# Kernel optimization log

Measured on AMD Instinct MI355X. Metric: run time of the kernel, lower is better.

The kernel has to match this reference:

```python
import jax, jax.numpy as jnp
import numpy as np

H = 4096          # hidden_size
I = 11008         # intermediate_size
G = 128           # AWQ group_size
# AWQ interleaved nibble order within each packed int32
_ORDER = jnp.array([0, 4, 1, 5, 2, 6, 3, 7], dtype=jnp.int32) * 4


def _mk_lin(key, K, N):
    k1, k2, k3 = jax.random.split(key, 3)
    qw = jax.random.randint(k1, (K, N // 8), 0, 100, dtype=jnp.int32)
    qz = jax.random.randint(k2, (K // G, N // 8), 0, 100, dtype=jnp.int32)
    sc = jax.random.normal(k3, (K // G, N), dtype=jnp.float32) * 0.02
    return qw, qz, sc


def setup_inputs() -> dict:
    key = jax.random.key(0)
    ks = jax.random.split(key, 7)
    x = jax.random.normal(ks[0], (8, 16, H), dtype=jnp.float32)
    ln1_w = jnp.ones((H,), dtype=jnp.float32)
    ln2_w = jnp.ones((H,), dtype=jnp.float32)
    qkv_qw, qkv_qz, qkv_sc = _mk_lin(ks[1], H, 3 * H)
    o_qw, o_qz, o_sc = _mk_lin(ks[2], H, H)
    gu_qw, gu_qz, gu_sc = _mk_lin(ks[3], H, 2 * I)
    dn_qw, dn_qz, dn_sc = _mk_lin(ks[4], I, H)
    return dict(x=x, ln1_w=ln1_w, ln2_w=ln2_w,
                qkv_qw=qkv_qw, qkv_qz=qkv_qz, qkv_sc=qkv_sc,
                o_qw=o_qw, o_qz=o_qz, o_sc=o_sc,
                gu_qw=gu_qw, gu_qz=gu_qz, gu_sc=gu_sc,
                dn_qw=dn_qw, dn_qz=dn_qz, dn_sc=dn_sc)


def rmsnorm(x, w, eps=1e-6):
    return x * jax.lax.rsqrt(jnp.mean(x * x, axis=-1, keepdims=True) + eps) * w


def dequant(qw, qz, sc):
    # qw: [K, N//8] int32 -> [K, N]; qz: [K//G, N//8] -> [K//G, N]
    K = qw.shape[0]
    N = sc.shape[1]
    w = ((qw[:, :, None] >> _ORDER) & 0xF).reshape(K, N).astype(sc.dtype)
    z = ((qz[:, :, None] >> _ORDER) & 0xF).reshape(K // G, N).astype(sc.dtype)
    return (w - jnp.repeat(z, G, axis=0)) * jnp.repeat(sc, G, axis=0)


def lite_linear(x, qw, qz, sc):
    return x @ dequant(qw, qz, sc)


def reference(x, ln1_w, ln2_w,
              qkv_qw, qkv_qz, qkv_sc,
              o_qw, o_qz, o_sc,
              gu_qw, gu_qz, gu_sc,
              dn_qw, dn_qz, dn_sc):
    residual = x
    h = rmsnorm(x, ln1_w)
    h = lite_linear(h, qkv_qw, qkv_qz, qkv_sc)[..., :H]  # mock attn: take q slice
    h = lite_linear(h, o_qw, o_qz, o_sc)
    h = residual + h
    residual = h
    h = rmsnorm(h, ln2_w)
    gate_up = lite_linear(h, gu_qw, gu_qz, gu_sc)
    gate, up = gate_up[..., :I], gate_up[..., I:]
    h = lite_linear(jax.nn.silu(gate) * up, dn_qw, dn_qz, dn_sc)
    return residual + h
```

## Files before the change

### kernel.cpp

```cpp
#include <hip/hip_runtime.h>

typedef unsigned int   u32;
typedef unsigned short u16;

typedef _Float16 h2  __attribute__((ext_vector_type(2)));
typedef _Float16 h8  __attribute__((ext_vector_type(8)));
typedef float    f32x4 __attribute__((ext_vector_type(4)));

#define M_TOK 128

__device__ __forceinline__ u16 f2h_(float f) {
    _Float16 h = (_Float16)f; return __builtin_bit_cast(u16, h);
}
__device__ __forceinline__ float h2f_(u16 b) {
    _Float16 h = __builtin_bit_cast(_Float16, b); return (float)h;
}
__device__ __forceinline__ void acc8(uint4 v, float* s) {
#pragma unroll
    for (int i = 0; i < 4; ++i) {
        u32 w = ((const u32*)&v)[i];
        s[2 * i]     += h2f_((u16)(w & 0xFFFF));
        s[2 * i + 1] += h2f_((u16)(w >> 16));
    }
}

__constant__ int SHC[8] = {0, 16, 4, 20, 8, 24, 12, 28};

__launch_bounds__(256)
__global__ void pack_zs(const int* __restrict__ qz, const float* __restrict__ sc,
                        u32* __restrict__ zs, int qws, int scs, int Ncols, int total) {
    const int idx = blockIdx.x * 256 + threadIdx.x;
    if (idx >= total) return;
    const int g = idx / Ncols, n = idx - g * Ncols;
    const u32 d = (u32)qz[(size_t)g * qws + (n >> 3)];
    const u32 zj = (d >> SHC[n & 7]) & 15u;
    const u32 mz = 0xE400u | zj;
    const u16 sh = f2h_(sc[(size_t)g * scs + n]);
    zs[(size_t)g * Ncols + n] = mz | ((u32)sh << 16);
}


__launch_bounds__(256)
__global__ void rmsnorm_k(const float* __restrict__ in, const float* __restrict__ w,
                          u16* __restrict__ out) {
    const int row = blockIdx.x;
    const float* x = in + (size_t)row * 4096;
    float ss = 0.f;
#pragma unroll
    for (int j = 0; j < 16; ++j) {
        float v = x[threadIdx.x + 256 * j];
        ss += v * v;
    }
#pragma unroll
    for (int off = 32; off > 0; off >>= 1) ss += __shfl_down(ss, off, 64);
    __shared__ float ws4[4];
    if ((threadIdx.x & 63) == 0) ws4[threadIdx.x >> 6] = ss;
    __syncthreads();
    float total = ws4[0] + ws4[1] + ws4[2] + ws4[3];
    float r = rsqrtf(total * (1.f / 4096.f) + 1e-6f);
    const int mt = row >> 4, l16 = row & 15;
#pragma unroll
    for (int c2 = 0; c2 < 2; ++c2) {
        int c = threadIdx.x * 2 + c2;
        int kb = c >> 2, qq = c & 3;
        u16 o8[8];
#pragma unroll
        for (int j = 0; j < 8; ++j) {
            int i = c * 8 + j;
            o8[j] = f2h_(x[i] * r * w[i]);
        }
        *(uint4*)(out + ((size_t)(kb * 8 + mt) * 64 + qq * 16 + l16) * 8) = *(const uint4*)o8;
    }
}

__launch_bounds__(256, 3)
__global__ void gemm_awq(const u16* __restrict__ A, const u32* __restrict__ zs,
                         const int* __restrict__ qw, u16* __restrict__ part,
                         int qws, int N, int K, int kchunk) {
    __shared__ __align__(16) char ldsB[4 * 9216];

    const int tid = threadIdx.x, w = tid >> 6, lane = tid & 63;
    const int q = lane >> 4, l16 = lane & 15;
    const int nwg = gridDim.x, bid = blockIdx.x;
    const int qq8 = nwg >> 3, r8 = nwg & 7, xcd = bid & 7, boff = bid >> 3;
    const int bx = (xcd < r8 ? xcd * (qq8 + 1) : r8 * (qq8 + 1) + (xcd - r8) * qq8) + boff;
    const int n0w = bx * 128 + w * 32;
    const int pc0 = n0w >> 3;
    const int kp = lane & 31, h = lane >> 5;
    const int sk = blockIdx.y, kc0 = sk * kchunk, kend = min(kc0 + kchunk, K);

    char* buf0 = ldsB + w * 9216;
    char* buf1 = buf0 + 4608;
    const u16* Ala = A + lane * 8;
    const int* qws_base = qw + pc0;
    const u32* zsA = zs + n0w + h * 8;
    const u32* zsB = zs + n0w + 16 + h * 8;

    f32x4 acc[8][2] = {};
    uint4 za0, za1, zb0, zb1;

    auto ldraw = [&](int k0) -> uint4 {
        return *(const uint4*)(qws_base + (size_t)(k0 + lane) * qws);
    };
    auto loadzs = [&](int g) {
        za0 = *(const uint4*)(zsA + (size_t)g * N);
        za1 = *(const uint4*)(zsA + (size_t)g * N + 4);
        zb0 = *(const uint4*)(zsB + (size_t)g * N);
        zb1 = *(const uint4*)(zsB + (size_t)g * N + 4);
    };
    auto dq = [&](uint4 rv, char* buf) {
        const int i0 = kp * 8, i1 = i0 + 4;
        int b00 = __builtin_amdgcn_ds_bpermute(i0, (int)rv.x);
        int b10 = __builtin_amdgcn_ds_bpermute(i0, (int)rv.y);
        int b20 = __builtin_amdgcn_ds_bpermute(i0, (int)rv.z);
        int b30 = __builtin_amdgcn_ds_bpermute(i0, (int)rv.w);
        int b01 = __builtin_amdgcn_ds_bpermute(i1, (int)rv.x);
        int b11 = __builtin_amdgcn_ds_bpermute(i1, (int)rv.y);
        int b21 = __builtin_amdgcn_ds_bpermute(i1, (int)rv.z);
        int b31 = __builtin_amdgcn_ds_bpermute(i1, (int)rv.w);
        u32 qd0 = (u32)(h ? b10 : b00);
        u32 qd1 = (u32)(h ? b11 : b01);
        u32 qd2 = (u32)(h ? b30 : b20);
        u32 qd3 = (u32)(h ? b31 : b21);
        auto emit8 = [&](u32 w0, u32 w1, int nb, uint4 z0, uint4 z1) {
            char* bb = buf + kp * 4 + nb * 144;
            u32 w0s = w0 >> 4, w1s = w1 >> 4;
            auto em = [&](int j, u32 a0, u32 a1, int b, u32 zsj) {
                h2 mz = __builtin_bit_cast(h2, __builtin_amdgcn_perm(zsj, zsj, 0x01000100u));
                h2 s2 = __builtin_bit_cast(h2, __builtin_amdgcn_perm(zsj, zsj, 0x03020302u));
                u32 t = __builtin_amdgcn_perm(a1, a0, (u32)(b | ((b + 4) << 16)));
                u32 u = (t & 0x000F000Fu) | 0x64006400u;
                h2 v = (__builtin_bit_cast(h2, u) + mz) * s2;
                *(u32*)(bb + j * 144) = __builtin_bit_cast(u32, v);
            };
            em(0, w0, w1, 0, z0.x);  em(4, w0, w1, 1, z1.x);
            em(1, w0, w1, 2, z0.y);  em(5, w0, w1, 3, z1.y);
            em(2, w0s, w1s, 0, z0.z); em(6, w0s, w1s, 1, z1.z);
            em(3, w0s, w1s, 2, z0.w); em(7, w0s, w1s, 3, z1.w);
        };
        emit8(qd0, qd1, h * 8, za0, za1);
        emit8(qd2, qd3, 16 + h * 8, zb0, zb1);
    };

    uint4 rv_n = {0, 0, 0, 0};

    loadzs(kc0 >> 7);
    uint4 rv0 = ldraw(kc0);
    if (kc0 + 64 < kend) rv_n = ldraw(kc0 + 64);
    dq(rv0, buf0);
    if (((kc0 + 64) & 127) == 0 && kc0 + 64 < kend)
        loadzs((kc0 + 64) >> 7);

    char* cur = buf0; char* nxt = buf1;
    for (int k0 = kc0; k0 < kend; k0 += 64) {
        const bool kn1 = (k0 + 64) < kend, kn2 = (k0 + 128) < kend;
        uint4 rv_f = {0, 0, 0, 0};
        if (kn2) rv_f = ldraw(k0 + 128);
        if (kn1) dq(rv_n, nxt);
        if (kn2 && (((k0 + 128) & 127) == 0))
            loadzs((k0 + 128) >> 7);
        const int kb = k0 >> 5;
#pragma unroll
        for (int c = 0; c < 2; ++c) {
            uint4 bvc[2];
#pragma unroll
            for (int nt = 0; nt < 2; ++nt)
                bvc[nt] = *(const uint4*)(cur + (nt * 16 + l16) * 144 + c * 64 + q * 16);
            uint4 afc[8];
#pragma unroll
            for (int mt = 0; mt < 8; ++mt)
                afc[mt] = *(const uint4*)(Ala + (size_t)((kb + c) * 8 + mt) * 512);
#pragma unroll
            for (int mt = 0; mt < 8; ++mt)
#pragma unroll
                for (int nt = 0; nt < 2; ++nt)
                    acc[mt][nt] = __builtin_amdgcn_mfma_f32_16x16x32_f16(
                        __builtin_bit_cast(h8, afc[mt]),
                        __builtin_bit_cast(h8, bvc[nt]),
                        acc[mt][nt], 0, 0, 0);
        }
        rv_n = rv_f;
        char* t = cur; cur = nxt; nxt = t;
    }

    u16* pp = part + (size_t)sk * M_TOK * N;
#pragma unroll
    for (int mt = 0; mt < 8; ++mt)
#pragma unroll
        for (int nt = 0; nt < 2; ++nt) {
            const int n = n0w + nt * 16 + l16;
#pragma unroll
            for (int r = 0; r < 4; ++r) {
                const int m = mt * 16 + q * 4 + r;
                pp[(size_t)m * N + n] = f2h_(acc[mt][nt][r]);
            }
        }
}

__launch_bounds__(256)
__global__ void reduce_to_afrag(const u16* __restrict__ part, u16* __restrict__ out,
                                int SK) {
    const int idx = blockIdx.x * 256 + threadIdx.x;
    const int m = idx >> 9, c = idx & 511;
    float s[8] = {};
    for (int k = 0; k < SK; ++k)
        acc8(*(const uint4*)(part + (size_t)k * 524288 + (size_t)m * 4096 + c * 8), s);
    const int kb = c >> 2, qq = c & 3, mt = m >> 4, l16 = m & 15;
    u16 o8[8];
#pragma unroll
    for (int j = 0; j < 8; ++j) o8[j] = f2h_(s[j]);
    *(uint4*)(out + ((size_t)(kb * 8 + mt) * 64 + qq * 16 + l16) * 8) = *(const uint4*)o8;
}

__launch_bounds__(256)
__global__ void reduce_add_f32(const u16* __restrict__ part, const float* __restrict__ resin,
                               float* __restrict__ out, int SK) {
    const int idx = blockIdx.x * 256 + threadIdx.x;
    const size_t base = (size_t)idx * 8;
    float s[8];
    *(float4*)&s[0] = *(const float4*)(resin + base);
    *(float4*)&s[4] = *(const float4*)(resin + base + 4);
    for (int k = 0; k < SK; ++k)
        acc8(*(const uint4*)(part + (size_t)k * 524288 + base), s);
    *(float4*)(out + base)     = *(const float4*)&s[0];
    *(float4*)(out + base + 4) = *(const float4*)&s[4];
}

__launch_bounds__(256)
__global__ void silu_mul(const u16* __restrict__ part, u16* __restrict__ act, int SK) {
    const int idx = blockIdx.x * 256 + threadIdx.x;
    const int m = idx / 1376, c = idx - m * 1376;
    const int nb = c * 8;
    float g[8] = {}, u[8] = {};
    for (int k = 0; k < SK; ++k) {
        const size_t base = (size_t)k * 2818048 + (size_t)m * 22016 + nb;
        acc8(*(const uint4*)(part + base), g);
        acc8(*(const uint4*)(part + base + 11008), u);
    }
    const int kb = nb >> 5, qq = (nb >> 3) & 3, mt = m >> 4, l16 = m & 15;
    u16 o8[8];
#pragma unroll
    for (int j = 0; j < 8; ++j) {
        float a = g[j] / (1.f + __expf(-g[j])) * u[j];
        o8[j] = f2h_(a);
    }
    *(uint4*)(act + ((size_t)(kb * 8 + mt) * 64 + qq * 16 + l16) * 8) = *(const uint4*)o8;
}

extern "C" void kernel_launch(void* const* d_in, const int* in_sizes, int n_in,
                              void* d_out, int out_size, void* d_ws, size_t ws_size,
                              hipStream_t stream) {
    const float* x      = (const float*)d_in[0];
    const float* ln1_w  = (const float*)d_in[1];
    const float* ln2_w  = (const float*)d_in[2];
    const int*   qkv_qw = (const int*)d_in[3];
    const int*   qkv_qz = (const int*)d_in[4];
    const float* qkv_sc = (const float*)d_in[5];
    const int*   o_qw   = (const int*)d_in[6];
    const int*   o_qz   = (const int*)d_in[7];
    const float* o_sc   = (const float*)d_in[8];
    const int*   gu_qw  = (const int*)d_in[9];
    const int*   gu_qz  = (const int*)d_in[10];
    const float* gu_sc  = (const float*)d_in[11];
    const int*   dn_qw  = (const int*)d_in[12];
    const int*   dn_qz  = (const int*)d_in[13];
    const float* dn_sc  = (const float*)d_in[14];
    float* out = (float*)d_out;

    char* ws = (char*)d_ws;
    u16*   pbuf = (u16*)(ws);
    u32*   zsb  = (u32*)(ws + 22544384);
    u16*   act  = (u16*)(ws + 25362432);
    float* res2 = (float*)(ws + 28180480);
    u16*   slot = (u16*)(ws + 30277632);

    rmsnorm_k<<<128, 256, 0, stream>>>(x, ln1_w, slot);
    pack_zs<<<512, 256, 0, stream>>>(qkv_qz, qkv_sc, zsb, 1536, 12288, 4096, 131072);

    gemm_awq<<<dim3(32, 16), 256, 0, stream>>>(slot, zsb, qkv_qw, pbuf,
                                               1536, 4096, 4096, 256);
    reduce_to_afrag<<<256, 256, 0, stream>>>(pbuf, slot, 16);
    pack_zs<<<512, 256, 0, stream>>>(o_qz, o_sc, zsb, 512, 4096, 4096, 131072);

    gemm_awq<<<dim3(32, 16), 256, 0, stream>>>(slot, zsb, o_qw, pbuf,
                                               512, 4096, 4096, 256);
    reduce_add_f32<<<256, 256, 0, stream>>>(pbuf, x, res2, 16);

    rmsnorm_k<<<128, 256, 0, stream>>>(res2, ln2_w, slot);
    pack_zs<<<2752, 256, 0, stream>>>(gu_qz, gu_sc, zsb, 2752, 22016, 22016, 704512);

    gemm_awq<<<dim3(172, 4), 256, 0, stream>>>(slot, zsb, gu_qw, pbuf,
                                               2752, 22016, 4096, 1024);
    silu_mul<<<688, 256, 0, stream>>>(pbuf, act, 4);
    pack_zs<<<1376, 256, 0, stream>>>(dn_qz, dn_sc, zsb, 512, 4096, 4096, 352256);

    gemm_awq<<<dim3(32, 20), 256, 0, stream>>>(act, zsb, dn_qw, pbuf,
                                               512, 4096, 11008, 576);
    reduce_add_f32<<<256, 256, 0, stream>>>(pbuf, res2, out, 20);
}
```

Measured before the change: 311.2 us.

## Split M across waves, deepen weight prefetch, and retune split-K for AWQ GEMMs

Adds a template mode in which each workgroup covers 64 columns, with waves split over the two halves of the 128 tokens, so each wave keeps 4 M-tiles instead of 8. This cuts accumulator registers, allows higher occupancy, and doubles the workgroup count for the 4096-wide GEMMs. The main loop now loads weights three steps ahead, issues the B-fragment LDS reads and the bpermutes before the MFMAs, and raises wave priority during the MFMA block. Dequantisation emission is moved after the math so it overlaps. The gate/up GEMM doubles its split-K count, which requires a larger partial buffer and shifts the workspace offsets, in exchange for more reduction traffic in silu_mul.

```diff
diff --git a/kernel.cpp b/kernel.cpp
--- a/kernel.cpp
+++ b/kernel.cpp
@@ -73,18 +73,21 @@
     }
 }
 
-__launch_bounds__(256, 3)
+template<int MSPLIT>
+__launch_bounds__(256, MSPLIT == 2 ? 4 : 3)
 __global__ void gemm_awq(const u16* __restrict__ A, const u32* __restrict__ zs,
                          const int* __restrict__ qw, u16* __restrict__ part,
                          int qws, int N, int K, int kchunk) {
+    constexpr int MT = (MSPLIT == 2) ? 4 : 8;
     __shared__ __align__(16) char ldsB[4 * 9216];
 
     const int tid = threadIdx.x, w = tid >> 6, lane = tid & 63;
     const int q = lane >> 4, l16 = lane & 15;
+    const int mh = (MSPLIT == 2) ? (w >> 1) : 0;
     const int nwg = gridDim.x, bid = blockIdx.x;
     const int qq8 = nwg >> 3, r8 = nwg & 7, xcd = bid & 7, boff = bid >> 3;
     const int bx = (xcd < r8 ? xcd * (qq8 + 1) : r8 * (qq8 + 1) + (xcd - r8) * qq8) + boff;
-    const int n0w = bx * 128 + w * 32;
+    const int n0w = (MSPLIT == 2) ? (bx * 64 + (w & 1) * 32) : (bx * 128 + w * 32);
     const int pc0 = n0w >> 3;
     const int kp = lane & 31, h = lane >> 5;
     const int sk = blockIdx.y, kc0 = sk * kchunk, kend = min(kc0 + kchunk, K);
@@ -96,7 +99,7 @@
     const u32* zsA = zs + n0w + h * 8;
     const u32* zsB = zs + n0w + 16 + h * 8;
 
-    f32x4 acc[8][2] = {};
+    f32x4 acc[MT][2] = {};
     uint4 za0, za1, zb0, zb1;
 
     auto ldraw = [&](int k0) -> uint4 {
@@ -108,27 +111,29 @@
         zb0 = *(const uint4*)(zsB + (size_t)g * N);
         zb1 = *(const uint4*)(zsB + (size_t)g * N + 4);
     };
-    auto dq = [&](uint4 rv, char* buf) {
+    auto bperm8 = [&](uint4 rv, int* b) {
         const int i0 = kp * 8, i1 = i0 + 4;
-        int b00 = __builtin_amdgcn_ds_bpermute(i0, (int)rv.x);
-        int b10 = __builtin_amdgcn_ds_bpermute(i0, (int)rv.y);
-        int b20 = __builtin_amdgcn_ds_bpermute(i0, (int)rv.z);
-        int b30 = __builtin_amdgcn_ds_bpermute(i0, (int)rv.w);
-        int b01 = __builtin_amdgcn_ds_bpermute(i1, (int)rv.x);
-        int b11 = __builtin_amdgcn_ds_bpermute(i1, (int)rv.y);
-        int b21 = __builtin_amdgcn_ds_bpermute(i1, (int)rv.z);
-        int b31 = __builtin_amdgcn_ds_bpermute(i1, (int)rv.w);
-        u32 qd0 = (u32)(h ? b10 : b00);
-        u32 qd1 = (u32)(h ? b11 : b01);
-        u32 qd2 = (u32)(h ? b30 : b20);
-        u32 qd3 = (u32)(h ? b31 : b21);
+        b[0] = __builtin_amdgcn_ds_bpermute(i0, (int)rv.x);
+        b[1] = __builtin_amdgcn_ds_bpermute(i0, (int)rv.y);
+        b[2] = __builtin_amdgcn_ds_bpermute(i0, (int)rv.z);
+        b[3] = __builtin_amdgcn_ds_bpermute(i0, (int)rv.w);
+        b[4] = __builtin_amdgcn_ds_bpermute(i1, (int)rv.x);
+        b[5] = __builtin_amdgcn_ds_bpermute(i1, (int)rv.y);
+        b[6] = __builtin_amdgcn_ds_bpermute(i1, (int)rv.z);
+        b[7] = __builtin_amdgcn_ds_bpermute(i1, (int)rv.w);
+    };
+    auto emit_all = [&](const int* b, char* buf) {
+        u32 qd0 = (u32)(h ? b[1] : b[0]);
+        u32 qd1 = (u32)(h ? b[5] : b[4]);
+        u32 qd2 = (u32)(h ? b[3] : b[2]);
+        u32 qd3 = (u32)(h ? b[7] : b[6]);
         auto emit8 = [&](u32 w0, u32 w1, int nb, uint4 z0, uint4 z1) {
             char* bb = buf + kp * 4 + nb * 144;
             u32 w0s = w0 >> 4, w1s = w1 >> 4;
-            auto em = [&](int j, u32 a0, u32 a1, int b, u32 zsj) {
+            auto em = [&](int j, u32 a0, u32 a1, int bsel, u32 zsj) {
                 h2 mz = __builtin_bit_cast(h2, __builtin_amdgcn_perm(zsj, zsj, 0x01000100u));
                 h2 s2 = __builtin_bit_cast(h2, __builtin_amdgcn_perm(zsj, zsj, 0x03020302u));
-                u32 t = __builtin_amdgcn_perm(a1, a0, (u32)(b | ((b + 4) << 16)));
+                u32 t = __builtin_amdgcn_perm(a1, a0, (u32)(bsel | ((bsel + 4) << 16)));
                 u32 u = (t & 0x000F000Fu) | 0x64006400u;
                 h2 v = (__builtin_bit_cast(h2, u) + mz) * s2;
                 *(u32*)(bb + j * 144) = __builtin_bit_cast(u32, v);
@@ -142,56 +147,66 @@
         emit8(qd2, qd3, 16 + h * 8, zb0, zb1);
     };
 
-    uint4 rv_n = {0, 0, 0, 0};
-
     loadzs(kc0 >> 7);
     uint4 rv0 = ldraw(kc0);
-    if (kc0 + 64 < kend) rv_n = ldraw(kc0 + 64);
-    dq(rv0, buf0);
+    uint4 rv_n = {0, 0, 0, 0}, rv_nn = {0, 0, 0, 0};
+    if (kc0 + 64 < kend)  rv_n  = ldraw(kc0 + 64);
+    if (kc0 + 128 < kend) rv_nn = ldraw(kc0 + 128);
+    {
+        int bp0[8];
+        bperm8(rv0, bp0);
+        emit_all(bp0, buf0);
+    }
     if (((kc0 + 64) & 127) == 0 && kc0 + 64 < kend)
         loadzs((kc0 + 64) >> 7);
 
     char* cur = buf0; char* nxt = buf1;
+    int bp[8];
     for (int k0 = kc0; k0 < kend; k0 += 64) {
-        const bool kn1 = (k0 + 64) < kend, kn2 = (k0 + 128) < kend;
-        uint4 rv_f = {0, 0, 0, 0};
-        if (kn2) rv_f = ldraw(k0 + 128);
-        if (kn1) dq(rv_n, nxt);
-        if (kn2 && (((k0 + 128) & 127) == 0))
-            loadzs((k0 + 128) >> 7);
+        const bool kn1 = (k0 + 64) < kend, kn3 = (k0 + 192) < kend;
+        uint4 bv[2][2];
+#pragma unroll
+        for (int c = 0; c < 2; ++c)
+#pragma unroll
+            for (int nt = 0; nt < 2; ++nt)
+                bv[c][nt] = *(const uint4*)(cur + (nt * 16 + l16) * 144 + c * 64 + q * 16);
+        if (kn1) bperm8(rv_n, bp);
         const int kb = k0 >> 5;
+        __builtin_amdgcn_s_setprio(1);
 #pragma unroll
         for (int c = 0; c < 2; ++c) {
-            uint4 bvc[2];
-#pragma unroll
-            for (int nt = 0; nt < 2; ++nt)
-                bvc[nt] = *(const uint4*)(cur + (nt * 16 + l16) * 144 + c * 64 + q * 16);
-            uint4 afc[8];
-#pragma unroll
-            for (int mt = 0; mt < 8; ++mt)
-                afc[mt] = *(const uint4*)(Ala + (size_t)((kb + c) * 8 + mt) * 512);
-#pragma unroll
-            for (int mt = 0; mt < 8; ++mt)
+            uint4 afc[MT];
+#pragma unroll
+            for (int mt = 0; mt < MT; ++mt)
+                afc[mt] = *(const uint4*)(Ala + (size_t)((kb + c) * 8 + mh * MT + mt) * 512);
+#pragma unroll
+            for (int mt = 0; mt < MT; ++mt)
 #pragma unroll
                 for (int nt = 0; nt < 2; ++nt)
                     acc[mt][nt] = __builtin_amdgcn_mfma_f32_16x16x32_f16(
                         __builtin_bit_cast(h8, afc[mt]),
-                        __builtin_bit_cast(h8, bvc[nt]),
+                        __builtin_bit_cast(h8, bv[c][nt]),
                         acc[mt][nt], 0, 0, 0);
         }
-        rv_n = rv_f;
+        __builtin_amdgcn_s_setprio(0);
+        uint4 rv_f = {0, 0, 0, 0};
+        if (kn3) rv_f = ldraw(k0 + 192);
+        if (kn1) emit_all(bp, nxt);
+        if (((k0 + 128) & 127) == 0 && (k0 + 128) < kend)
+            loadzs((k0 + 128) >> 7);
+        rv_n = rv_nn; rv_nn = rv_f;
         char* t = cur; cur = nxt; nxt = t;
     }
 
     u16* pp = part + (size_t)sk * M_TOK * N;
 #pragma unroll
-    for (int mt = 0; mt < 8; ++mt)
+    for (int mt = 0; mt < MT; ++mt)
 #pragma unroll
         for (int nt = 0; nt < 2; ++nt) {
             const int n = n0w + nt * 16 + l16;
 #pragma unroll
             for (int r = 0; r < 4; ++r) {
-                const int m = mt * 16 + q * 4 + r;
+                const int m = (mh * MT + mt) * 16 + q * 4 + r;
                 pp[(size_t)m * N + n] = f2h_(acc[mt][nt][r]);
             }
         }
@@ -269,32 +284,32 @@
 
     char* ws = (char*)d_ws;
     u16*   pbuf = (u16*)(ws);
-    u32*   zsb  = (u32*)(ws + 22544384);
-    u16*   act  = (u16*)(ws + 25362432);
-    float* res2 = (float*)(ws + 28180480);
-    u16*   slot = (u16*)(ws + 30277632);
+    u32*   zsb  = (u32*)(ws + 45088768);
+    u16*   act  = (u16*)(ws + 47906816);
+    float* res2 = (float*)(ws + 50724864);
+    u16*   slot = (u16*)(ws + 52822016);
 
     rmsnorm_k<<<128, 256, 0, stream>>>(x, ln1_w, slot);
     pack_zs<<<512, 256, 0, stream>>>(qkv_qz, qkv_sc, zsb, 1536, 12288, 4096, 131072);
 
-    gemm_awq<<<dim3(32, 16), 256, 0, stream>>>(slot, zsb, qkv_qw, pbuf,
-                                               1536, 4096, 4096, 256);
+    gemm_awq<2><<<dim3(64, 16), 256, 0, stream>>>(slot, zsb, qkv_qw, pbuf,
+                                                  1536, 4096, 4096, 256);
     reduce_to_afrag<<<256, 256, 0, stream>>>(pbuf, slot, 16);
     pack_zs<<<512, 256, 0, stream>>>(o_qz, o_sc, zsb, 512, 4096, 4096, 131072);
 
-    gemm_awq<<<dim3(32, 16), 256, 0, stream>>>(slot, zsb, o_qw, pbuf,
-                                               512, 4096, 4096, 256);
+    gemm_awq<2><<<dim3(64, 16), 256, 0, stream>>>(slot, zsb, o_qw, pbuf,
+                                                  512, 4096, 4096, 256);
     reduce_add_f32<<<256, 256, 0, stream>>>(pbuf, x, res2, 16);
 
     rmsnorm_k<<<128, 256, 0, stream>>>(res2, ln2_w, slot);
     pack_zs<<<2752, 256, 0, stream>>>(gu_qz, gu_sc, zsb, 2752, 22016, 22016, 704512);
 
-    gemm_awq<<<dim3(172, 4), 256, 0, stream>>>(slot, zsb, gu_qw, pbuf,
-                                               2752, 22016, 4096, 1024);
-    silu_mul<<<688, 256, 0, stream>>>(pbuf, act, 4);
+    gemm_awq<1><<<dim3(172, 8), 256, 0, stream>>>(slot, zsb, gu_qw, pbuf,
+                                                  2752, 22016, 4096, 512);
+    silu_mul<<<688, 256, 0, stream>>>(pbuf, act, 8);
     pack_zs<<<1376, 256, 0, stream>>>(dn_qz, dn_sc, zsb, 512, 4096, 4096, 352256);
 
-    gemm_awq<<<dim3(32, 20), 256, 0, stream>>>(act, zsb, dn_qw, pbuf,
-                                               512, 4096, 11008, 576);
+    gemm_awq<2><<<dim3(64, 20), 256, 0, stream>>>(act, zsb, dn_qw, pbuf,
+                                                  512, 4096, 11008, 576);
     reduce_add_f32<<<256, 256, 0, stream>>>(pbuf, res2, out, 20);
 }
```

Result: slower. 318.7 us (+2.4%).
